# Performance work log

Hardware: AMD Instinct MI355X
Metric: run time of the kernel (lower is better)

## Reference

```python
import jax, jax.numpy as jnp
import numpy as np

DIM = 2048
HEAD = 256
SEQ = 4096

def setup_inputs() -> dict:
    key = jax.random.key(0)
    ks = jax.random.split(key, 7)
    s = 1.0 / np.sqrt(DIM)
    return {
        "marketStateBatch": jax.random.normal(ks[0], (SEQ, DIM), dtype=jnp.float32),
        "Wq": jax.random.uniform(ks[1], (HEAD, DIM), jnp.float32, -s, s),
        "bq": jax.random.uniform(ks[2], (HEAD,), jnp.float32, -s, s),
        "Wk": jax.random.uniform(ks[3], (HEAD, DIM), jnp.float32, -s, s),
        "bk": jax.random.uniform(ks[4], (HEAD,), jnp.float32, -s, s),
        "Wv": jax.random.uniform(ks[5], (HEAD, DIM), jnp.float32, -s, s),
        "bv": jax.random.uniform(ks[6], (HEAD,), jnp.float32, -s, s),
    }

def reference(marketStateBatch, Wq, bq, Wk, bk, Wv, bv):
    x = marketStateBatch  # [S, D]
    q = x @ Wq.T + bq     # [S, H]
    k = x @ Wk.T + bk     # [S, H]
    v = x @ Wv.T + bv     # [S, H]
    # NOTE: original scales by sqrt(dimensionSize), the INPUT dim, not head dim.
    scores = (q @ k.T) * (1.0 / np.sqrt(DIM))  # [S, S]
    S = x.shape[0]
    causal = jnp.tril(jnp.ones((S, S), dtype=bool))
    scores = jnp.where(causal, scores, -jnp.inf)
    attn = jax.nn.softmax(scores, axis=-1)
    # torch.nan_to_num(attn, 0.0): rows are never all -inf here (diag kept),
    # but replicate the op faithfully.
    attn = jnp.nan_to_num(attn, nan=0.0)
    return attn @ v  # [S, H]
```

## Files before the change

### kernel.cpp

```cpp
#include <hip/hip_runtime.h>
#include <stdint.h>

#define SEQ 4096
#define DIMK 2048
#define HD 256

typedef __attribute__((ext_vector_type(8))) short bf16x8;
typedef __attribute__((ext_vector_type(4))) short u16x4;
typedef __attribute__((ext_vector_type(4))) float f32x4;
typedef __attribute__((ext_vector_type(16))) float f32x16;
typedef unsigned short u16;
typedef unsigned int u32;

#define BAR() asm volatile("s_barrier" ::: "memory")
#define VMCNT(n) asm volatile("s_waitcnt vmcnt(" #n ")" ::: "memory")

__device__ __forceinline__ u16 f2bf(float f) {
    u32 u = __float_as_uint(f);
    u += 0x7FFFu + ((u >> 16) & 1u);
    return (u16)(u >> 16);
}

__device__ __forceinline__ float bf2f(u16 h) {
    u32 u = ((u32)h) << 16;
    return __uint_as_float(u);
}

__device__ __forceinline__ bf16x8 pack8(f32x4 a0, f32x4 a1) {
    bf16x8 v8;
    v8[0]=(short)f2bf(a0[0]); v8[1]=(short)f2bf(a0[1]);
    v8[2]=(short)f2bf(a0[2]); v8[3]=(short)f2bf(a0[3]);
    v8[4]=(short)f2bf(a1[0]); v8[5]=(short)f2bf(a1[1]);
    v8[6]=(short)f2bf(a1[2]); v8[7]=(short)f2bf(a1[3]);
    return v8;
}

__device__ __forceinline__ void gl16(const void* g, void* l) {
    __builtin_amdgcn_global_load_lds(
        (const __attribute__((address_space(1))) void*)g,
        (__attribute__((address_space(3))) void*)l, 16, 0, 0);
}

__device__ __forceinline__ u32 cvtpk(float lo, float hi) {
    u32 d;
    asm("v_cvt_pk_bf16_f32 %0, %1, %2" : "=v"(d) : "v"(lo), "v"(hi));
    return d;
}

__device__ __forceinline__ void plswap(u32& x, u32& y) {
#if __has_builtin(__builtin_amdgcn_permlane32_swap)
    typedef int i32x2 __attribute__((ext_vector_type(2)));
    i32x2 r = __builtin_amdgcn_permlane32_swap((int)x, (int)y, false, false);
    x = (u32)r[0]; y = (u32)r[1];
#else
    asm("v_permlane32_swap_b32 %0, %1" : "+v"(x), "+v"(y));
#endif
}

__global__ __launch_bounds__(256) void cvt_all2(
    const float* __restrict__ x, const float* __restrict__ Wq,
    const float* __restrict__ Wk, const float* __restrict__ Wv,
    u16* __restrict__ xb_sw, u16* __restrict__ wb_sw)
{
    const int y = blockIdx.y;
    int i = blockIdx.x * 256 + threadIdx.x;
    int stride = gridDim.x * 256;
    if (y == 0) {
        for (; i < SEQ*DIMK/8; i += stride) {
            int row = i >> 8, c8 = i & 255;
            f32x4 a0 = *(const f32x4*)(x + (size_t)row*DIMK + c8*8);
            f32x4 a1 = *(const f32x4*)(x + (size_t)row*DIMK + c8*8 + 4);
            int mt = row >> 6, rl = row & 63, kt = c8 >> 3, sl = c8 & 7;
            size_t dst = ((size_t)(mt*32 + kt))*4096 + rl*64 + ((sl ^ (rl&7))*8);
            *(bf16x8*)(xb_sw + dst) = pack8(a0, a1);
        }
    } else {
        const float* W = (y==1) ? Wq : (y==2) ? Wk : Wv;
        for (; i < HD*DIMK/8; i += stride) {
            int row = i >> 8, c8 = i & 255;
            f32x4 a0 = *(const f32x4*)(W + (size_t)row*DIMK + c8*8);
            f32x4 a1 = *(const f32x4*)(W + (size_t)row*DIMK + c8*8 + 4);
            int gr = (y-1)*256 + row;
            int nt = gr >> 7, rl = gr & 127, kt = c8 >> 3, sl = c8 & 7;
            size_t dst = ((size_t)(nt*32 + kt))*8192 + rl*64 + ((sl ^ (rl&7))*8);
            *(bf16x8*)(wb_sw + dst) = pack8(a0, a1);
        }
    }
}

__global__ __launch_bounds__(256, 2) void qkv_gemm2b(
    const u16* __restrict__ xb_sw, const u16* __restrict__ wb_sw,
    const float* __restrict__ bq, const float* __restrict__ bk,
    const float* __restrict__ bv,
    u16* __restrict__ qb, u16* __restrict__ kb_t, u16* __restrict__ vt_t)
{
    __shared__ char T[3][24576];

    const int tid = threadIdx.x;
    const int lane = tid & 63;
    const int w = tid >> 6;
    const int r = lane & 15, g = lane >> 4;
    const int wr = w >> 1, wc = w & 1;
    const int mt = blockIdx.x;
    const int y  = blockIdx.y;
    const int z  = y >> 1;
    const float* bias = (z==0) ? bq : (z==1) ? bk : bv;

    const u16* abase = xb_sw + (size_t)mt*32*4096;
    const u16* bbase = wb_sw + (size_t)y*32*8192;

    f32x4 zero = {0.f,0.f,0.f,0.f};
    f32x4 acc[2][4];
    #pragma unroll
    for (int m = 0; m < 2; ++m)
        #pragma unroll
        for (int n = 0; n < 4; ++n) acc[m][n] = zero;

    auto stage = [&](int b, int kt) {
        const u16* ag = abase + (size_t)kt*4096 + w*1024 + lane*8;
        const u16* bg = bbase + (size_t)kt*8192 + w*2048 + lane*8;
        char* al = T[b] + w*2048;
        char* bl = T[b] + 8192 + w*4096;
        gl16(ag,        al);
        gl16(ag + 512,  al + 1024);
        gl16(bg,        bl);
        gl16(bg + 512,  bl + 1024);
        gl16(bg + 1024, bl + 2048);
        gl16(bg + 1536, bl + 3072);
    };

    stage(0, 0);
    stage(1, 1);

    for (int kt = 0; kt < 32; ++kt) {
        if (kt < 31) { VMCNT(6); } else { VMCNT(0); }
        BAR();
        if (kt + 2 < 32) stage((kt + 2) % 3, kt + 2);
        const char* A = T[kt % 3];
        const char* B = T[kt % 3] + 8192;
        __builtin_amdgcn_s_setprio(1);
        #pragma unroll
        for (int kc = 0; kc < 2; ++kc) {
            bf16x8 af[2], bfr[4];
            #pragma unroll
            for (int m = 0; m < 2; ++m) {
                int arow = wr*32 + m*16 + r;
                af[m] = *(const bf16x8*)(A + arow*128 + (((kc*4+g) ^ (arow&7)) << 4));
            }
            #pragma unroll
            for (int n = 0; n < 4; ++n) {
                int brow = wc*64 + n*16 + r;
                bfr[n] = *(const bf16x8*)(B + brow*128 + (((kc*4+g) ^ (brow&7)) << 4));
            }
            #pragma unroll
            for (int m = 0; m < 2; ++m)
                #pragma unroll
                for (int n = 0; n < 4; ++n)
                    acc[m][n] = __builtin_amdgcn_mfma_f32_16x16x32_bf16(
                        af[m], bfr[n], acc[m][n], 0, 0, 0);
        }
        __builtin_amdgcn_s_setprio(0);
    }

    const int m0 = mt*64, n0 = y*128;
    const float qs = 0.03187936f;
    if (z == 0) {
        #pragma unroll
        for (int n = 0; n < 4; ++n) {
            int hc = (n0 + wc*64 + n*16 + r) & 255;
            float bcol = bias[hc];
            #pragma unroll
            for (int m = 0; m < 2; ++m) {
                int row0 = m0 + wr*32 + m*16 + g*4;
                #pragma unroll
                for (int j = 0; j < 4; ++j)
                    qb[(size_t)(row0+j)*HD + hc] = f2bf((acc[m][n][j] + bcol) * qs);
            }
        }
    } else if (z == 1) {
        #pragma unroll
        for (int n = 0; n < 4; ++n) {
            int hc = (n0 + wc*64 + n*16 + r) & 255;
            float bcol = bias[hc];
            #pragma unroll
            for (int m = 0; m < 2; ++m) {
                int row0 = m0 + wr*32 + m*16 + g*4;
                #pragma unroll
                for (int j = 0; j < 4; ++j) {
                    int rowj = row0 + j;
                    int t = rowj >> 5, rl = rowj & 31;
                    kb_t[(size_t)t*8192 + rl*256 + (((hc>>3) ^ (rl&7))*8) + (hc&7)]
                        = f2bf(acc[m][n][j] + bcol);
                }
            }
        }
    } else {
        #pragma unroll
        for (int n = 0; n < 4; ++n) {
            int hc = (n0 + wc*64 + n*16 + r) & 255;
            float bcol = bias[hc];
            #pragma unroll
            for (int m = 0; m < 2; ++m) {
                int kv0 = m0 + wr*32 + m*16 + g*4;
                int t = kv0 >> 5, kl = kv0 & 31;
                u16x4 pk;
                #pragma unroll
                for (int j = 0; j < 4; ++j) pk[j] = (short)f2bf(acc[m][n][j] + bcol);
                *(u16x4*)(vt_t + (size_t)t*8192 + hc*32 +
                          (((kl>>3) ^ (hc&3) ^ ((hc>>2)&3))*8) + (kl&7)) = pk;
            }
        }
    }
}

__global__ __launch_bounds__(256, 2) void attn_part6(
    const u16* __restrict__ qb, const u16* __restrict__ kb_t,
    const u16* __restrict__ vt_t,
    u16* __restrict__ po, float* __restrict__ pm, float* __restrict__ pl,
    int C)
{
    __shared__ char Kb[2][16384];
    __shared__ char Vb[2][16384];

    const int pid = blockIdx.x;
    int Q = 0, a0 = 0;
    for (int k = 0; k < 32; ++k) {
        int nsk = (4*k + 4 + C - 1) / C;
        if (pid < a0 + nsk) { Q = k; break; }
        a0 += nsk;
    }
    const int s  = pid - a0;
    const int nt = 4*Q + 4;
    const int t0 = s*C;
    const int t1 = min(t0 + C, nt);

    const int tid = threadIdx.x;
    const int L = tid & 63;
    const int w = tid >> 6;
    const int l31 = L & 31;
    const int h   = L >> 5;
    const int qg  = Q*128 + w*32 + l31;
    const int vsw = (l31 & 3) ^ ((l31 >> 2) & 3);
    const int kx  = l31 & 7;

    auto stage = [&](int t, int b) {
        const u16* kg = kb_t + (size_t)t*8192 + w*2048 + L*8;
        const u16* vg = vt_t + (size_t)t*8192 + w*2048 + L*8;
        char* kl = Kb[b] + w*4096;
        char* vl = Vb[b] + w*4096;
        #pragma unroll
        for (int i = 0; i < 4; ++i) gl16(kg + i*512, kl + i*1024);
        #pragma unroll
        for (int i = 0; i < 4; ++i) gl16(vg + i*512, vl + i*1024);
    };

    stage(t0, t0 & 1);
    if (t0 + 1 < t1) stage(t0 + 1, (t0 + 1) & 1);
    else             stage(t0,     (t0 + 1) & 1);

    bf16x8 qf[16];
    {
        const u16* qp = qb + (size_t)qg*HD + h*8;
        #pragma unroll
        for (int c = 0; c < 16; ++c) qf[c] = *(const bf16x8*)(qp + c*16);
    }

    f32x16 o[8];
    #pragma unroll
    for (int ht = 0; ht < 8; ++ht)
        #pragma unroll
        for (int e = 0; e < 16; ++e) o[ht][e] = 0.f;
    float mrun = -1e30f, lrun = 0.f;

    for (int t = t0; t < t1; ++t) {
        if (t + 1 < t1) { VMCNT(8); } else { VMCNT(0); }
        BAR();
        const char* K = Kb[t & 1];
        const char* V = Vb[t & 1];

        #define LDK(c) (*(const bf16x8*)(K + l31*512 + (((2*(c) + h) ^ kx) << 4)))
        f32x16 sv;
        #pragma unroll
        for (int e = 0; e < 16; ++e) sv[e] = 0.f;
        __builtin_amdgcn_s_setprio(1);
        {
            bf16x8 ka = LDK(0), kb_ = LDK(1), kc = LDK(2), kd = LDK(3);
            sv = __builtin_amdgcn_mfma_f32_32x32x16_bf16(ka,  qf[0],  sv, 0,0,0); ka  = LDK(4);
            sv = __builtin_amdgcn_mfma_f32_32x32x16_bf16(kb_, qf[1],  sv, 0,0,0); kb_ = LDK(5);
            sv = __builtin_amdgcn_mfma_f32_32x32x16_bf16(kc,  qf[2],  sv, 0,0,0); kc  = LDK(6);
            sv = __builtin_amdgcn_mfma_f32_32x32x16_bf16(kd,  qf[3],  sv, 0,0,0); kd  = LDK(7);
            sv = __builtin_amdgcn_mfma_f32_32x32x16_bf16(ka,  qf[4],  sv, 0,0,0); ka  = LDK(8);
            sv = __builtin_amdgcn_mfma_f32_32x32x16_bf16(kb_, qf[5],  sv, 0,0,0); kb_ = LDK(9);
            sv = __builtin_amdgcn_mfma_f32_32x32x16_bf16(kc,  qf[6],  sv, 0,0,0); kc  = LDK(10);
            sv = __builtin_amdgcn_mfma_f32_32x32x16_bf16(kd,  qf[7],  sv, 0,0,0); kd  = LDK(11);
            sv = __builtin_amdgcn_mfma_f32_32x32x16_bf16(ka,  qf[8],  sv, 0,0,0); ka  = LDK(12);
            sv = __builtin_amdgcn_mfma_f32_32x32x16_bf16(kb_, qf[9],  sv, 0,0,0); kb_ = LDK(13);
            sv = __builtin_amdgcn_mfma_f32_32x32x16_bf16(kc,  qf[10], sv, 0,0,0); kc  = LDK(14);
            sv = __builtin_amdgcn_mfma_f32_32x32x16_bf16(kd,  qf[11], sv, 0,0,0); kd  = LDK(15);
            sv = __builtin_amdgcn_mfma_f32_32x32x16_bf16(ka,  qf[12], sv, 0,0,0);
            sv = __builtin_amdgcn_mfma_f32_32x32x16_bf16(kb_, qf[13], sv, 0,0,0);
            sv = __builtin_amdgcn_mfma_f32_32x32x16_bf16(kc,  qf[14], sv, 0,0,0);
            sv = __builtin_amdgcn_mfma_f32_32x32x16_bf16(kd,  qf[15], sv, 0,0,0);
        }
        #undef LDK
        __builtin_amdgcn_s_setprio(0);

        if (t*32 + 31 > Q*128 + w*32) {
            #pragma unroll
            for (int e = 0; e < 16; ++e) {
                int kvr = (e & 3) + 8*(e >> 2) + 4*h;
                if (t*32 + kvr > qg) sv[e] = -__builtin_inff();
            }
        }

        float m0_ = fmaxf(fmaxf(sv[0],sv[1]),  fmaxf(sv[2],sv[3]));
        float m1_ = fmaxf(fmaxf(sv[4],sv[5]),  fmaxf(sv[6],sv[7]));
        float m2_ = fmaxf(fmaxf(sv[8],sv[9]),  fmaxf(sv[10],sv[11]));
        float m3_ = fmaxf(fmaxf(sv[12],sv[13]),fmaxf(sv[14],sv[15]));
        float mx = fmaxf(fmaxf(m0_,m1_), fmaxf(m2_,m3_));
        mx = fmaxf(mx, __shfl_xor(mx, 32));
        if (__any(mx > mrun + 8.0f)) {
            float mnew  = fmaxf(mrun, mx);
            float alpha = exp2f(mrun - mnew);
            lrun *= alpha;
            #pragma unroll
            for (int ht = 0; ht < 8; ++ht) o[ht] *= alpha;
            mrun = mnew;
        }
        #pragma unroll
        for (int e = 0; e < 16; ++e) sv[e] = exp2f(sv[e] - mrun);
        float r0 = ((sv[0]+sv[1])+(sv[2]+sv[3])) + ((sv[4]+sv[5])+(sv[6]+sv[7]));
        float r1 = ((sv[8]+sv[9])+(sv[10]+sv[11])) + ((sv[12]+sv[13])+(sv[14]+sv[15]));
        float rs = r0 + r1;
        rs += __shfl_xor(rs, 32);
        lrun += rs;

        union { u32 wd[4]; bf16x8 v8; } up0, up1;
        {
            u32 A = cvtpk(sv[0],  sv[1]),  B = cvtpk(sv[2],  sv[3]);
            u32 Cc= cvtpk(sv[4],  sv[5]),  D = cvtpk(sv[6],  sv[7]);
            plswap(A, Cc); plswap(B, D);
            up0.wd[0]=A; up0.wd[1]=B; up0.wd[2]=Cc; up0.wd[3]=D;
            u32 A1 = cvtpk(sv[8],  sv[9]),  B1 = cvtpk(sv[10], sv[11]);
            u32 C1 = cvtpk(sv[12], sv[13]), D1 = cvtpk(sv[14], sv[15]);
            plswap(A1, C1); plswap(B1, D1);
            up1.wd[0]=A1; up1.wd[1]=B1; up1.wd[2]=C1; up1.wd[3]=D1;
        }
        bf16x8 pa0 = up0.v8, pa1 = up1.v8;

        __builtin_amdgcn_s_setprio(1);
        #pragma unroll
        for (int ht = 0; ht < 8; ++ht) {
            const char* vrow = V + (ht*32 + l31)*64;
            bf16x8 vf0 = *(const bf16x8*)(vrow + (((h)     ^ vsw) << 4));
            bf16x8 vf1 = *(const bf16x8*)(vrow + (((2 + h) ^ vsw) << 4));
            o[ht] = __builtin_amdgcn_mfma_f32_32x32x16_bf16(vf0, pa0, o[ht], 0, 0, 0);
            o[ht] = __builtin_amdgcn_mfma_f32_32x32x16_bf16(vf1, pa1, o[ht], 0, 0, 0);
        }
        __builtin_amdgcn_s_setprio(0);

        BAR();
        stage(min(t + 2, t1 - 1), t & 1);
    }

    VMCNT(0);

    if (h == 0) {
        pm[(size_t)pid*128 + w*32 + l31] = mrun;
        pl[(size_t)pid*128 + w*32 + l31] = lrun;
    }
    u16* op = po + ((size_t)pid*128 + w*32 + l31) * 256;
    #pragma unroll
    for (int ht = 0; ht < 8; ++ht)
        #pragma unroll
        for (int j = 0; j < 8; ++j) {
            u32 pk = (u32)f2bf(o[ht][2*j]) | ((u32)f2bf(o[ht][2*j+1]) << 16);
            int hdb = ht*32 + (j & 1)*2 + (j >> 1)*8 + 4*h;
            *(u32*)(op + hdb) = pk;
        }
}

__global__ __launch_bounds__(256) void attn_combine5(
    const u16* __restrict__ po, const float* __restrict__ pm,
    const float* __restrict__ pl, float* __restrict__ out, int C)
{
    const int tid = threadIdx.x;
    const int row = blockIdx.x * 16 + (tid >> 4);
    const int cg  = tid & 15;
    const int Q   = row >> 7, rr = row & 127;
    const int nt  = 4*Q + 4;
    const int ns  = (nt + C - 1) / C;
    int pid0 = 0;
    for (int k = 0; k < Q; ++k) pid0 += (4*k + 4 + C - 1) / C;

    float M = -1e30f;
    for (int s = 0; s < ns; ++s)
        M = fmaxf(M, pm[(size_t)(pid0+s)*128 + rr]);

    float lt = 0.f;
    f32x4 acc[4];
    f32x4 zero = {0.f,0.f,0.f,0.f};
    #pragma unroll
    for (int v = 0; v < 4; ++v) acc[v] = zero;

    for (int s = 0; s < ns; ++s) {
        float ms  = pm[(size_t)(pid0+s)*128 + rr];
        float wgt = exp2f(ms - M);
        lt += wgt * pl[(size_t)(pid0+s)*128 + rr];
        const u16* p = po + ((size_t)(pid0+s)*128 + rr)*256 + cg*16;
        #pragma unroll
        for (int v = 0; v < 4; ++v) {
            u16x4 pv = *(const u16x4*)(p + v*4);
            #pragma unroll
            for (int e = 0; e < 4; ++e)
                acc[v][e] += wgt * bf2f((u16)pv[e]);
        }
    }
    float inv = 1.f / lt;
    f32x4* op = (f32x4*)(out + (size_t)row*256 + cg*16);
    #pragma unroll
    for (int v = 0; v < 4; ++v) op[v] = acc[v] * inv;
}

extern "C" void kernel_launch(void* const* d_in, const int* in_sizes, int n_in,
                              void* d_out, int out_size, void* d_ws, size_t ws_size,
                              hipStream_t stream) {
    const float* x  = (const float*)d_in[0];
    const float* Wq = (const float*)d_in[1];
    const float* bq = (const float*)d_in[2];
    const float* Wk = (const float*)d_in[3];
    const float* bk = (const float*)d_in[4];
    const float* Wv = (const float*)d_in[5];
    const float* bv = (const float*)d_in[6];
    float* out = (float*)d_out;

    const size_t xb_bytes  = (size_t)SEQ * DIMK * 2;
    const size_t wb_bytes  = (size_t)768 * DIMK * 2;
    const size_t qkv_bytes = (size_t)SEQ * HD * 2;
    const size_t base = xb_bytes + wb_bytes + 3*qkv_bytes;

    int C = 64;
    size_t npid = 0;
    const int cand[4] = {5, 8, 16, 64};
    for (int ci = 0; ci < 4; ++ci) {
        int c = cand[ci];
        size_t np = 0;
        for (int k = 0; k < 32; ++k) np += (size_t)(4*k + 4 + c - 1) / c;
        size_t need = base + np * ((size_t)128*256*2 + 2*128*4);
        if (need <= ws_size) { C = c; npid = np; break; }
        if (ci == 3) { C = c; npid = np; }
    }

    char* p = (char*)d_ws;
    u16* xb_sw = (u16*)p; p += xb_bytes;
    u16* wb_sw = (u16*)p; p += wb_bytes;
    u16* qbuf  = (u16*)p; p += qkv_bytes;
    u16* kb_t  = (u16*)p; p += qkv_bytes;
    u16* vt_t  = (u16*)p; p += qkv_bytes;
    u16* po    = (u16*)p; p += npid * 128 * 256 * 2;
    float* pm  = (float*)p; p += npid * 128 * 4;
    float* pl  = (float*)p; p += npid * 128 * 4;

    cvt_all2<<<dim3(512, 4), 256, 0, stream>>>(x, Wq, Wk, Wv, xb_sw, wb_sw);

    qkv_gemm2b<<<dim3(SEQ/64, 6), 256, 0, stream>>>(
        xb_sw, wb_sw, bq, bk, bv, qbuf, kb_t, vt_t);

    attn_part6<<<(int)npid, 256, 0, stream>>>(
        qbuf, kb_t, vt_t, po, pm, pl, C);

    attn_combine5<<<SEQ/16, 256, 0, stream>>>(po, pm, pl, out, C);
}
```

Measured before the change: 78.58 us.

## Process two KV tiles per iteration with split K/V staging in attention

Result: slower. 81.36 us (+3.5%).

```diff
diff --git a/kernel.cpp b/kernel.cpp
--- a/kernel.cpp
+++ b/kernel.cpp
@@ -213,7 +213,7 @@
     }
 }
 
-__global__ __launch_bounds__(256, 2) void attn_part6(
+__global__ __launch_bounds__(256, 2) void attn_part7(
     const u16* __restrict__ qb, const u16* __restrict__ kb_t,
     const u16* __restrict__ vt_t,
     u16* __restrict__ po, float* __restrict__ pm, float* __restrict__ pl,
@@ -243,20 +243,21 @@
     const int vsw = (l31 & 3) ^ ((l31 >> 2) & 3);
     const int kx  = l31 & 7;
 
-    auto stage = [&](int t, int b) {
+    auto stageK = [&](int t, int b) {
         const u16* kg = kb_t + (size_t)t*8192 + w*2048 + L*8;
+        char* kl = Kb[b] + w*4096;
+        #pragma unroll
+        for (int i = 0; i < 4; ++i) gl16(kg + i*512, kl + i*1024);
+    };
+    auto stageV = [&](int t, int b) {
         const u16* vg = vt_t + (size_t)t*8192 + w*2048 + L*8;
-        char* kl = Kb[b] + w*4096;
         char* vl = Vb[b] + w*4096;
-        #pragma unroll
-        for (int i = 0; i < 4; ++i) gl16(kg + i*512, kl + i*1024);
         #pragma unroll
         for (int i = 0; i < 4; ++i) gl16(vg + i*512, vl + i*1024);
     };
 
-    stage(t0, t0 & 1);
-    if (t0 + 1 < t1) stage(t0 + 1, (t0 + 1) & 1);
-    else             stage(t0,     (t0 + 1) & 1);
+    stageK(t0, 0); stageK(t0 + 1, 1);
+    stageV(t0, 0); stageV(t0 + 1, 1);
 
     bf16x8 qf[16];
     {
@@ -272,52 +273,73 @@
         for (int e = 0; e < 16; ++e) o[ht][e] = 0.f;
     float mrun = -1e30f, lrun = 0.f;
 
-    for (int t = t0; t < t1; ++t) {
-        if (t + 1 < t1) { VMCNT(8); } else { VMCNT(0); }
+    for (int t = t0; t < t1; t += 2) {
+        VMCNT(8);
         BAR();
-        const char* K = Kb[t & 1];
-        const char* V = Vb[t & 1];
-
-        #define LDK(c) (*(const bf16x8*)(K + l31*512 + (((2*(c) + h) ^ kx) << 4)))
-        f32x16 sv;
-        #pragma unroll
-        for (int e = 0; e < 16; ++e) sv[e] = 0.f;
+        const char* KA  = Kb[0];
+        const char* KB_ = Kb[1];
+
+        #define LDKA(c) (*(const bf16x8*)(KA  + l31*512 + (((2*(c) + h) ^ kx) << 4)))
+        #define LDKB(c) (*(const bf16x8*)(KB_ + l31*512 + (((2*(c) + h) ^ kx) << 4)))
+        f32x16 sa, sb;
+        #pragma unroll
+        for (int e = 0; e < 16; ++e) { sa[e] = 0.f; sb[e] = 0.f; }
         __builtin_amdgcn_s_setprio(1);
         {
-            bf16x8 ka = LDK(0), kb_ = LDK(1), kc = LDK(2), kd = LDK(3);
-            sv = __builtin_amdgcn_mfma_f32_32x32x16_bf16(ka,  qf[0],  sv, 0,0,0); ka  = LDK(4);
-            sv = __builtin_amdgcn_mfma_f32_32x32x16_bf16(kb_, qf[1],  sv, 0,0,0); kb_ = LDK(5);
-            sv = __builtin_amdgcn_mfma_f32_32x32x16_bf16(kc,  qf[2],  sv, 0,0,0); kc  = LDK(6);
-            sv = __builtin_amdgcn_mfma_f32_32x32x16_bf16(kd,  qf[3],  sv, 0,0,0); kd  = LDK(7);
-            sv = __builtin_amdgcn_mfma_f32_32x32x16_bf16(ka,  qf[4],  sv, 0,0,0); ka  = LDK(8);
-            sv = __builtin_amdgcn_mfma_f32_32x32x16_bf16(kb_, qf[5],  sv, 0,0,0); kb_ = LDK(9);
-            sv = __builtin_amdgcn_mfma_f32_32x32x16_bf16(kc,  qf[6],  sv, 0,0,0); kc  = LDK(10);
-            sv = __builtin_amdgcn_mfma_f32_32x32x16_bf16(kd,  qf[7],  sv, 0,0,0); kd  = LDK(11);
-            sv = __builtin_amdgcn_mfma_f32_32x32x16_bf16(ka,  qf[8],  sv, 0,0,0); ka  = LDK(12);
-            sv = __builtin_amdgcn_mfma_f32_32x32x16_bf16(kb_, qf[9],  sv, 0,0,0); kb_ = LDK(13);
-            sv = __builtin_amdgcn_mfma_f32_32x32x16_bf16(kc,  qf[10], sv, 0,0,0); kc  = LDK(14);
-            sv = __builtin_amdgcn_mfma_f32_32x32x16_bf16(kd,  qf[11], sv, 0,0,0); kd  = LDK(15);
-            sv = __builtin_amdgcn_mfma_f32_32x32x16_bf16(ka,  qf[12], sv, 0,0,0);
-            sv = __builtin_amdgcn_mfma_f32_32x32x16_bf16(kb_, qf[13], sv, 0,0,0);
-            sv = __builtin_amdgcn_mfma_f32_32x32x16_bf16(kc,  qf[14], sv, 0,0,0);
-            sv = __builtin_amdgcn_mfma_f32_32x32x16_bf16(kd,  qf[15], sv, 0,0,0);
-        }
-        #undef LDK
+            bf16x8 ka0 = LDKA(0), kb0 = LDKB(0), ka1 = LDKA(1), kb1 = LDKB(1);
+            #define STEP2(c0, c1, pc0, pc1)                                          \
+                sa = __builtin_amdgcn_mfma_f32_32x32x16_bf16(ka0, qf[c0], sa, 0,0,0);\
+                sb = __builtin_amdgcn_mfma_f32_32x32x16_bf16(kb0, qf[c0], sb, 0,0,0);\
+                if (pc0 < 16) { ka0 = LDKA(pc0); kb0 = LDKB(pc0); }                  \
+                sa = __builtin_amdgcn_mfma_f32_32x32x16_bf16(ka1, qf[c1], sa, 0,0,0);\
+                sb = __builtin_amdgcn_mfma_f32_32x32x16_bf16(kb1, qf[c1], sb, 0,0,0);\
+                if (pc1 < 16) { ka1 = LDKA(pc1); kb1 = LDKB(pc1); }
+            STEP2(0, 1, 2, 3)
+            STEP2(2, 3, 4, 5)
+            STEP2(4, 5, 6, 7)
+            STEP2(6, 7, 8, 9)
+            STEP2(8, 9, 10, 11)
+            STEP2(10, 11, 12, 13)
+            STEP2(12, 13, 14, 15)
+            STEP2(14, 15, 16, 16)
+            #undef STEP2
+        }
         __builtin_amdgcn_s_setprio(0);
+        #undef LDKA
+        #undef LDKB
+
+        BAR();
+        {
+            int kA2 = (t + 2 < t1) ? t + 2 : t1 - 1;
+            int kB2 = (t + 3 < t1) ? t + 3 : t1 - 1;
+            stageK(kA2, 0); stageK(kB2, 1);
+        }
 
         if (t*32 + 31 > Q*128 + w*32) {
             #pragma unroll
             for (int e = 0; e < 16; ++e) {
                 int kvr = (e & 3) + 8*(e >> 2) + 4*h;
-                if (t*32 + kvr > qg) sv[e] = -__builtin_inff();
-            }
-        }
-
-        float m0_ = fmaxf(fmaxf(sv[0],sv[1]),  fmaxf(sv[2],sv[3]));
-        float m1_ = fmaxf(fmaxf(sv[4],sv[5]),  fmaxf(sv[6],sv[7]));
-        float m2_ = fmaxf(fmaxf(sv[8],sv[9]),  fmaxf(sv[10],sv[11]));
-        float m3_ = fmaxf(fmaxf(sv[12],sv[13]),fmaxf(sv[14],sv[15]));
-        float mx = fmaxf(fmaxf(m0_,m1_), fmaxf(m2_,m3_));
+                if (t*32 + kvr > qg) sa[e] = -__builtin_inff();
+            }
+        }
+        if ((t+1)*32 + 31 > Q*128 + w*32) {
+            #pragma unroll
+            for (int e = 0; e < 16; ++e) {
+                int kvr = (e & 3) + 8*(e >> 2) + 4*h;
+                if ((t+1)*32 + kvr > qg) sb[e] = -__builtin_inff();
+            }
+        }
+
+        float ma0 = fmaxf(fmaxf(sa[0],sa[1]),  fmaxf(sa[2],sa[3]));
+        float ma1 = fmaxf(fmaxf(sa[4],sa[5]),  fmaxf(sa[6],sa[7]));
+        float ma2 = fmaxf(fmaxf(sa[8],sa[9]),  fmaxf(sa[10],sa[11]));
+        float ma3 = fmaxf(fmaxf(sa[12],sa[13]),fmaxf(sa[14],sa[15]));
+        float mb0 = fmaxf(fmaxf(sb[0],sb[1]),  fmaxf(sb[2],sb[3]));
+        float mb1 = fmaxf(fmaxf(sb[4],sb[5]),  fmaxf(sb[6],sb[7]));
+        float mb2 = fmaxf(fmaxf(sb[8],sb[9]),  fmaxf(sb[10],sb[11]));
+        float mb3 = fmaxf(fmaxf(sb[12],sb[13]),fmaxf(sb[14],sb[15]));
+        float mx = fmaxf(fmaxf(fmaxf(ma0,ma1), fmaxf(ma2,ma3)),
+                         fmaxf(fmaxf(mb0,mb1), fmaxf(mb2,mb3)));
         mx = fmaxf(mx, __shfl_xor(mx, 32));
         if (__any(mx > mrun + 8.0f)) {
             float mnew  = fmaxf(mrun, mx);
@@ -328,39 +350,62 @@
             mrun = mnew;
         }
         #pragma unroll
-        for (int e = 0; e < 16; ++e) sv[e] = exp2f(sv[e] - mrun);
-        float r0 = ((sv[0]+sv[1])+(sv[2]+sv[3])) + ((sv[4]+sv[5])+(sv[6]+sv[7]));
-        float r1 = ((sv[8]+sv[9])+(sv[10]+sv[11])) + ((sv[12]+sv[13])+(sv[14]+sv[15]));
-        float rs = r0 + r1;
+        for (int e = 0; e < 16; ++e) { sa[e] = exp2f(sa[e] - mrun);
+                                       sb[e] = exp2f(sb[e] - mrun); }
+        float rs = (((sa[0]+sa[1])+(sa[2]+sa[3])) + ((sa[4]+sa[5])+(sa[6]+sa[7])))
+                 + (((sa[8]+sa[9])+(sa[10]+sa[11])) + ((sa[12]+sa[13])+(sa[14]+sa[15])))
+                 + (((sb[0]+sb[1])+(sb[2]+sb[3])) + ((sb[4]+sb[5])+(sb[6]+sb[7])))
+                 + (((sb[8]+sb[9])+(sb[10]+sb[11])) + ((sb[12]+sb[13])+(sb[14]+sb[15])));
         rs += __shfl_xor(rs, 32);
         lrun += rs;
 
-        union { u32 wd[4]; bf16x8 v8; } up0, up1;
+        union { u32 wd[4]; bf16x8 v8; } uA0, uA1, uB0, uB1;
         {
-            u32 A = cvtpk(sv[0],  sv[1]),  B = cvtpk(sv[2],  sv[3]);
-            u32 Cc= cvtpk(sv[4],  sv[5]),  D = cvtpk(sv[6],  sv[7]);
+            u32 A = cvtpk(sa[0], sa[1]),  B = cvtpk(sa[2], sa[3]);
+            u32 Cc= cvtpk(sa[4], sa[5]),  D = cvtpk(sa[6], sa[7]);
             plswap(A, Cc); plswap(B, D);
-            up0.wd[0]=A; up0.wd[1]=B; up0.wd[2]=Cc; up0.wd[3]=D;
-            u32 A1 = cvtpk(sv[8],  sv[9]),  B1 = cvtpk(sv[10], sv[11]);
-            u32 C1 = cvtpk(sv[12], sv[13]), D1 = cvtpk(sv[14], sv[15]);
+            uA0.wd[0]=A; uA0.wd[1]=B; uA0.wd[2]=Cc; uA0.wd[3]=D;
+            u32 A1 = cvtpk(sa[8], sa[9]),   B1 = cvtpk(sa[10], sa[11]);
+            u32 C1 = cvtpk(sa[12], sa[13]), D1 = cvtpk(sa[14], sa[15]);
             plswap(A1, C1); plswap(B1, D1);
-            up1.wd[0]=A1; up1.wd[1]=B1; up1.wd[2]=C1; up1.wd[3]=D1;
-        }
-        bf16x8 pa0 = up0.v8, pa1 = up1.v8;
+            uA1.wd[0]=A1; uA1.wd[1]=B1; uA1.wd[2]=C1; uA1.wd[3]=D1;
+            u32 A2 = cvtpk(sb[0], sb[1]),  B2 = cvtpk(sb[2], sb[3]);
+            u32 C2 = cvtpk(sb[4], sb[5]),  D2 = cvtpk(sb[6], sb[7]);
+            plswap(A2, C2); plswap(B2, D2);
+            uB0.wd[0]=A2; uB0.wd[1]=B2; uB0.wd[2]=C2; uB0.wd[3]=D2;
+            u32 A3 = cvtpk(sb[8], sb[9]),   B3 = cvtpk(sb[10], sb[11]);
+            u32 C3 = cvtpk(sb[12], sb[13]), D3 = cvtpk(sb[14], sb[15]);
+            plswap(A3, C3); plswap(B3, D3);
+            uB1.wd[0]=A3; uB1.wd[1]=B3; uB1.wd[2]=C3; uB1.wd[3]=D3;
+        }
+
+        VMCNT(8);
+        BAR();
+        const char* VA  = Vb[0];
+        const char* VB_ = Vb[1];
 
         __builtin_amdgcn_s_setprio(1);
         #pragma unroll
         for (int ht = 0; ht < 8; ++ht) {
-            const char* vrow = V + (ht*32 + l31)*64;
-            bf16x8 vf0 = *(const bf16x8*)(vrow + (((h)     ^ vsw) << 4));
-            bf16x8 vf1 = *(const bf16x8*)(vrow + (((2 + h) ^ vsw) << 4));
-            o[ht] = __builtin_amdgcn_mfma_f32_32x32x16_bf16(vf0, pa0, o[ht], 0, 0, 0);
-            o[ht] = __builtin_amdgcn_mfma_f32_32x32x16_bf16(vf1, pa1, o[ht], 0, 0, 0);
+            const char* vrowA = VA  + (ht*32 + l31)*64;
+            const char* vrowB = VB_ + (ht*32 + l31)*64;
+            bf16x8 va0 = *(const bf16x8*)(vrowA + (((h)     ^ vsw) << 4));
+            bf16x8 va1 = *(const bf16x8*)(vrowA + (((2 + h) ^ vsw) << 4));
+            bf16x8 vb0 = *(const bf16x8*)(vrowB + (((h)     ^ vsw) << 4));
+            bf16x8 vb1 = *(const bf16x8*)(vrowB + (((2 + h) ^ vsw) << 4));
+            o[ht] = __builtin_amdgcn_mfma_f32_32x32x16_bf16(va0, uA0.v8, o[ht], 0, 0, 0);
+            o[ht] = __builtin_amdgcn_mfma_f32_32x32x16_bf16(va1, uA1.v8, o[ht], 0, 0, 0);
+            o[ht] = __builtin_amdgcn_mfma_f32_32x32x16_bf16(vb0, uB0.v8, o[ht], 0, 0, 0);
+            o[ht] = __builtin_amdgcn_mfma_f32_32x32x16_bf16(vb1, uB1.v8, o[ht], 0, 0, 0);
         }
         __builtin_amdgcn_s_setprio(0);
 
         BAR();
-        stage(min(t + 2, t1 - 1), t & 1);
+        {
+            int vA2 = (t + 2 < t1) ? t + 2 : t1 - 1;
+            int vB2 = (t + 3 < t1) ? t + 3 : t1 - 1;
+            stageV(vA2, 0); stageV(vB2, 1);
+        }
     }
 
     VMCNT(0);
@@ -441,7 +486,7 @@
 
     int C = 64;
     size_t npid = 0;
-    const int cand[4] = {5, 8, 16, 64};
+    const int cand[4] = {6, 8, 16, 64};
     for (int ci = 0; ci < 4; ++ci) {
         int c = cand[ci];
         size_t np = 0;
@@ -466,7 +511,7 @@
     qkv_gemm2b<<<dim3(SEQ/64, 6), 256, 0, stream>>>(
         xb_sw, wb_sw, bq, bk, bv, qbuf, kb_t, vt_t);
 
-    attn_part6<<<(int)npid, 256, 0, stream>>>(
+    attn_part7<<<(int)npid, 256, 0, stream>>>(
         qbuf, kb_t, vt_t, po, pm, pl, C);
 
     attn_combine5<<<SEQ/16, 256, 0, stream>>>(po, pm, pl, out, C);
```
